# Optimization experiments

Hardware: AMD Instinct MI355X
Metric: run time of the kernel (lower is better)

Reference implementation:

```python
import jax, jax.numpy as jnp
import numpy as np

BN_EPS = 1e-5
INTERP_EPS = 1e-8


def setup_inputs() -> dict:
    key = jax.random.key(0)
    ks = jax.random.split(key, 8)
    B, N, S, D1, D2 = 8, 8192, 2048, 128, 256
    C_in, C_mid, C_out = D1 + D2, 256, 256
    return {
        "xyz1": jax.random.normal(ks[0], (B, 3, N), dtype=jnp.float32),
        "xyz2": jax.random.normal(ks[1], (B, 3, S), dtype=jnp.float32),
        "points1": jax.random.normal(ks[2], (B, D1, N), dtype=jnp.float32),
        "points2": jax.random.normal(ks[3], (B, D2, S), dtype=jnp.float32),
        "W0": jax.random.normal(ks[4], (C_mid, C_in), dtype=jnp.float32) * (1.0 / np.sqrt(C_in)),
        "b0": jnp.zeros((C_mid,), dtype=jnp.float32),
        "gamma0": jnp.ones((C_mid,), dtype=jnp.float32),
        "beta0": jnp.zeros((C_mid,), dtype=jnp.float32),
        "W1": jax.random.normal(ks[5], (C_out, C_mid), dtype=jnp.float32) * (1.0 / np.sqrt(C_mid)),
        "b1": jnp.zeros((C_out,), dtype=jnp.float32),
    }


def reference(xyz1, xyz2, points1, points2, W0, b0, gamma0, beta0, W1, b1):
    B, _, N = xyz1.shape
    S = xyz2.shape[2]
    x1 = jnp.transpose(xyz1, (0, 2, 1))  # (B, N, 3)
    x2 = jnpp = jnp.transpose(xyz2, (0, 2, 1))  # (B, S, 3)
    # squared distances: (B, N, S)
    d = (jnp.sum(x1 ** 2, -1)[:, :, None]
         + jnp.sum(x2 ** 2, -1)[:, None, :]
         - 2.0 * jnp.einsum('bnc,bsc->bns', x1, x2))
    # 3 nearest neighbors (fused top-3 instead of full sort; same math)
    neg_d, idx = jax.lax.top_k(-d, 3)  # (B, N, 3)
    dists = -neg_d
    recip = 1.0 / (dists + INTERP_EPS)
    weight = recip / jnp.sum(recip, axis=2, keepdims=True)  # (B, N, 3)
    p2t = jnp.transpose(points2, (0, 2, 1))  # (B, S, D2)
    D2 = p2t.shape[-1]
    gathered = jnp.take_along_axis(p2t, idx.reshape(B, N * 3, 1), axis=1).reshape(B, N, 3, D2)
    interp = jnp.einsum('bnkc,bnk->bcn', gathered, weight)  # (B, D2, N)
    new_points = jnp.concatenate([interp, points1], axis=1)  # (B, D2+D1, N)
    # conv0 (1x1) + BatchNorm (train mode, batch stats) + ReLU
    h = jnp.einsum('oc,bcn->bon', W0, new_points) + b0[None, :, None]
    mean = jnp.mean(h, axis=(0, 2), keepdims=True)
    var = jnp.mean((h - mean) ** 2, axis=(0, 2), keepdims=True)  # biased, as torch BN
    h = gamma0[None, :, None] * (h - mean) * jax.lax.rsqrt(var + BN_EPS) + beta0[None, :, None]
    h = jax.nn.relu(h)
    # conv1 (1x1) + Identity (module pairs conv1 with nn.Identity) + ReLU
    h = jnp.einsum('oc,bcn->bon', W1, h) + b1[None, :, None]
    return jax.nn.relu(h)
```

## Files before the change

kernel.cpp:

```cpp
#include <hip/hip_runtime.h>
#include <stdint.h>

constexpr int B = 8, N = 8192, S = 2048, D1 = 128, D2 = 256;
constexpr int CIN = 384, CMID = 256, COUT = 256;

typedef __attribute__((ext_vector_type(8))) _Float16 half8;
typedef __attribute__((ext_vector_type(4))) _Float16 half4;
typedef __attribute__((ext_vector_type(4))) float f32x4;

union HU { uint32_t u; _Float16 h[2]; };


__global__ __launch_bounds__(256) void k_top3(const float* __restrict__ xyz1,
                                              const float* __restrict__ xyz2,
                                              uint32_t* __restrict__ pw3) {
  __shared__ float4 Pq[S];
  __shared__ float md[4][3][128];
  __shared__ int mi[4][3][128];
  __shared__ float snrm[128];
  const int tid = threadIdx.x;
  const int wv = tid >> 6, lane = tid & 63;
  const int b = blockIdx.y;
  const int nb = blockIdx.x * 128;
  const float* x1 = xyz1 + (size_t)b * 3 * N;
  const float* x2 = xyz2 + (size_t)b * 3 * S;

  for (int j = tid; j < S; j += 256) {
    float sx = x2[j], sy = x2[j + S], sz = x2[j + 2 * S];
    Pq[j] = float4{sx, sy, sz, sx * sx + sy * sy + sz * sz};
  }
  float nax[2], nay[2], naz[2];
#pragma unroll
  for (int t = 0; t < 2; ++t) {
    const int n = nb + t * 64 + lane;
    const float ax = x1[n], ay = x1[n + N], az = x1[n + 2 * N];
    nax[t] = -2.f * ax; nay[t] = -2.f * ay; naz[t] = -2.f * az;
    if (wv == 0) snrm[t * 64 + lane] = ax * ax + ay * ay + az * az;
  }
  __syncthreads();

  float e0[2], e1[2], e2[2];
  int j0[2], j1[2], j2[2];
#pragma unroll
  for (int t = 0; t < 2; ++t) {
    e0[t] = 1e30f; e1[t] = 1e30f; e2[t] = 1e30f;
    j0[t] = 0; j1[t] = 0; j2[t] = 0;
  }
  const int s0 = wv * (S / 4), s1 = s0 + (S / 4);
#pragma unroll 4
  for (int s = s0; s < s1; ++s) {
    const float4 v = Pq[s];
#pragma unroll
    for (int t = 0; t < 2; ++t) {
      const float d = fmaf(nax[t], v.x, fmaf(nay[t], v.y, fmaf(naz[t], v.z, v.w)));
      const bool c0 = d < e0[t], c1 = d < e1[t], c2 = d < e2[t];
      const int u2 = c1 ? j1[t] : s;
      const int u1 = c0 ? j0[t] : s;
      j2[t] = c2 ? u2 : j2[t];
      j1[t] = c1 ? u1 : j1[t];
      j0[t] = c0 ? s : j0[t];
      e2[t] = __builtin_amdgcn_fmed3f(e1[t], e2[t], d);
      e1[t] = __builtin_amdgcn_fmed3f(e0[t], e1[t], d);
      e0[t] = fminf(e0[t], d);
    }
  }
#pragma unroll
  for (int t = 0; t < 2; ++t) {
    const int idx = t * 64 + lane;
    md[wv][0][idx] = e0[t]; mi[wv][0][idx] = j0[t];
    md[wv][1][idx] = e1[t]; mi[wv][1][idx] = j1[t];
    md[wv][2][idx] = e2[t]; mi[wv][2][idx] = j2[t];
  }
  __syncthreads();
  if (tid < 128) {
    float f0 = md[0][0][tid], f1 = md[0][1][tid], f2 = md[0][2][tid];
    int g0 = mi[0][0][tid], g1 = mi[0][1][tid], g2 = mi[0][2][tid];
#pragma unroll
    for (int w = 1; w < 4; ++w)
#pragma unroll
      for (int k = 0; k < 3; ++k) {
        float d = md[w][k][tid];
        int i = mi[w][k][tid];
        if (d < f2) {
          if (d < f1) {
            f2 = f1; g2 = g1;
            if (d < f0) { f1 = f0; g1 = g0; f0 = d; g0 = i; }
            else        { f1 = d;  g1 = i; }
          } else { f2 = d; g2 = i; }
        }
      }
    const float rn = snrm[tid];
    float q0 = fmaxf(f0 + rn, 0.f);
    float q1 = fmaxf(f1 + rn, 0.f);
    float q2 = fmaxf(f2 + rn, 0.f);
    float r0 = 1.0f / (q0 + 1e-8f), r1 = 1.0f / (q1 + 1e-8f), r2 = 1.0f / (q2 + 1e-8f);
    float inv = 1.0f / (r0 + r1 + r2);
    auto pack = [](int i, float w) -> uint32_t {
      uint32_t q = (uint32_t)(w * 2097152.0f + 0.5f);
      if (q > 0x1FFFFFu) q = 0x1FFFFFu;
      return ((uint32_t)i << 21) | q;
    };
    size_t base = ((size_t)b * N + nb + tid) * 3;
    pw3[base]     = pack(g0, r0 * inv);
    pw3[base + 1] = pack(g1, r1 * inv);
    pw3[base + 2] = pack(g2, r2 * inv);
  }
}

__global__ __launch_bounds__(256) void k_G(const float* __restrict__ points2,
                                           const float* __restrict__ W0,
                                           float* __restrict__ dout) {
  __shared__ half8 A_lds[4][256];
  __shared__ half8 B_lds[4][32];
  __shared__ float CT[32][258];
  const int tid = threadIdx.x;
  const int b = blockIdx.x >> 6;
  const int s0 = (blockIdx.x & 63) * 32;
  f32x4 acc[4][2] = {};
  const int wv = tid >> 6, lane = tid & 63;
  const int ln = lane & 15, quad = lane >> 4;
  const int bn = tid & 31, bkc = tid >> 5;
  const int ar = tid >> 3, ac4 = tid & 7;

  for (int kk = 0; kk < 256; kk += 32) {
    __syncthreads();
#pragma unroll
    for (int p = 0; p < 8; ++p) {
      int row = ar + 32 * p;
      const float4 v = *(const float4*)(W0 + (size_t)row * CIN + kk + ac4 * 4);
      half4 hv = {(_Float16)v.x, (_Float16)v.y, (_Float16)v.z, (_Float16)v.w};
      *(half4*)((_Float16*)&A_lds[ac4 >> 1][row] + (ac4 & 1) * 4) = hv;
    }
    {
      half4 hv;
#pragma unroll
      for (int j = 0; j < 4; ++j)
        hv[j] = (_Float16)points2[((size_t)(b * 256 + kk + bkc * 4 + j)) * S + s0 + bn];
      *(half4*)((_Float16*)&B_lds[bkc >> 1][bn] + (bkc & 1) * 4) = hv;
    }
    __syncthreads();
    half8 af[4], bf[2];
#pragma unroll
    for (int i = 0; i < 4; ++i) af[i] = A_lds[quad][wv * 64 + i * 16 + ln];
#pragma unroll
    for (int j = 0; j < 2; ++j) bf[j] = B_lds[quad][j * 16 + ln];
#pragma unroll
    for (int i = 0; i < 4; ++i)
#pragma unroll
      for (int j = 0; j < 2; ++j)
        acc[i][j] = __builtin_amdgcn_mfma_f32_16x16x32_f16(af[i], bf[j], acc[i][j], 0, 0, 0);
  }
  __syncthreads();
#pragma unroll
  for (int i = 0; i < 4; ++i)
#pragma unroll
    for (int reg = 0; reg < 4; ++reg) {
      int row = wv * 64 + i * 16 + quad * 4 + reg;
#pragma unroll
      for (int j = 0; j < 2; ++j) CT[j * 16 + ln][row] = acc[i][j][reg];
    }
  __syncthreads();
  const int sl = tid >> 3, g = tid & 7;
  float* g0 = dout + ((size_t)(b * 256 + 128)) * 8192 + (size_t)(s0 + sl) * 256 + g * 32;
#pragma unroll
  for (int q = 0; q < 8; ++q)
    *(float4*)(g0 + q * 4) = *(const float4*)&CT[sl][g * 32 + q * 4];
}

__global__ __launch_bounds__(256) void k_interp(const uint32_t* __restrict__ pw3,
                                                const float* __restrict__ dout_c,
                                                uint32_t* __restrict__ dout_u) {
  __shared__ int sidx[96];
  __shared__ float sw[96];
  const int tid = threadIdx.x;
  const int b = blockIdx.x >> 8;
  const int n0 = (blockIdx.x & 255) * 32;
  if (tid < 96) {
    uint32_t p = pw3[((size_t)b * N + n0) * 3 + tid];
    sidx[tid] = (int)(p >> 21);
    sw[tid] = (float)(p & 0x1FFFFFu) * (1.0f / 2097152.0f);
  }
  __syncthreads();
  const int colL = tid >> 3, p = tid & 7;
  const float* Gb = dout_c + ((size_t)(b * 256 + 128)) * 8192;
  float a[32];
#pragma unroll
  for (int q = 0; q < 32; ++q) a[q] = 0.f;
#pragma unroll
  for (int k = 0; k < 3; ++k) {
    int j = sidx[colL * 3 + k];
    float w = sw[colL * 3 + k];
    const float* g = Gb + (size_t)j * 256 + p * 32;
#pragma unroll
    for (int q = 0; q < 8; ++q) {
      float4 v = *(const float4*)(g + q * 4);
      a[q * 4 + 0] += w * v.x; a[q * 4 + 1] += w * v.y;
      a[q * 4 + 2] += w * v.z; a[q * 4 + 3] += w * v.w;
    }
  }
#pragma unroll
  for (int q = 0; q < 16; ++q) {
    int cp = p * 16 + q;
    HU u;
    u.h[0] = (_Float16)a[2 * q];
    u.h[1] = (_Float16)a[2 * q + 1];
    dout_u[((size_t)(b * 256 + cp)) * 8192 + n0 + colL] = u.u;
  }
}

__global__ __launch_bounds__(256) void k_wpack(const float* __restrict__ W0,
                                               const float* __restrict__ W1,
                                               _Float16* __restrict__ W1h,
                                               _Float16* __restrict__ W0h) {
  const int bid = blockIdx.x;
  if (bid < 64) {
    const int gid = bid * 256 + threadIdx.x;
    const float4 v = *(const float4*)(W1 + (size_t)gid * 4);
    half4 h = {(_Float16)v.x, (_Float16)v.y, (_Float16)v.z, (_Float16)v.w};
    *(half4*)(W1h + (size_t)gid * 4) = h;
  } else {
    const int gid = (bid - 64) * 256 + threadIdx.x;
    const int row = gid >> 5, c4 = gid & 31;
    const float4 v = *(const float4*)(W0 + (size_t)row * CIN + 256 + c4 * 4);
    half4 h = {(_Float16)v.x, (_Float16)v.y, (_Float16)v.z, (_Float16)v.w};
    *(half4*)(W0h + (size_t)row * 128 + c4 * 4) = h;
  }
}

__global__ __launch_bounds__(256) void k_h(uint32_t* __restrict__ h2,
                                           float* __restrict__ dpart,
                                           const float* __restrict__ points1,
                                           const _Float16* __restrict__ W0h,
                                           const float* __restrict__ b0) {
  __shared__ half8 B_lds[16][32];
  __shared__ float red_s[256], red_q[256], sb0[256];
  const int tid = threadIdx.x;
  const int b = blockIdx.x >> 8;
  const int cb = blockIdx.x & 255;
  const int n0 = cb * 32;
  sb0[tid] = b0[tid];
  const int wv = tid >> 6, lane = tid & 63;
  const int ln = lane & 15, quad = lane >> 4;

  f32x4 acc[4][2];
#pragma unroll
  for (int i = 0; i < 4; ++i) {
    const int rb = wv * 64 + i * 16 + quad * 4;
    const int cp0 = rb >> 1;
#pragma unroll
    for (int j = 0; j < 2; ++j) {
      const int col = n0 + j * 16 + ln;
      const size_t a0 = ((size_t)(b * 256 + cp0)) * 8192 + col;
      HU ua, ub;
      ua.u = h2[a0];
      ub.u = h2[a0 + 8192];
      acc[i][j][0] = (float)ua.h[0];
      acc[i][j][1] = (float)ua.h[1];
      acc[i][j][2] = (float)ub.h[0];
      acc[i][j][3] = (float)ub.h[1];
    }
  }
  {
    const int col = tid & 31;
    const int kc0 = tid >> 5;
#pragma unroll
    for (int it = 0; it < 2; ++it) {
      const int kc = kc0 + 8 * it;
      half8 hv;
#pragma unroll
      for (int j = 0; j < 8; ++j)
        hv[j] = (_Float16)points1[((size_t)(b * D1 + kc * 8 + j)) * N + n0 + col];
      B_lds[kc][col] = hv;
    }
  }
  __syncthreads();
  for (int kk = 0; kk < 128; kk += 32) {
    half8 af[4], bf[2];
#pragma unroll
    for (int i = 0; i < 4; ++i) {
      const int row = wv * 64 + i * 16 + ln;
      af[i] = *(const half8*)(W0h + (size_t)row * 128 + kk + quad * 8);
    }
#pragma unroll
    for (int j = 0; j < 2; ++j)
      bf[j] = B_lds[(kk >> 3) + quad][j * 16 + ln];
#pragma unroll
    for (int i = 0; i < 4; ++i)
#pragma unroll
      for (int j = 0; j < 2; ++j)
        acc[i][j] = __builtin_amdgcn_mfma_f32_16x16x32_f16(af[i], bf[j], acc[i][j], 0, 0, 0);
  }
#pragma unroll
  for (int i = 0; i < 4; ++i) {
    const int rb = wv * 64 + i * 16 + quad * 4;
    const int cp0 = rb >> 1;
    float rs[4] = {0.f, 0.f, 0.f, 0.f}, rq[4] = {0.f, 0.f, 0.f, 0.f};
#pragma unroll
    for (int j = 0; j < 2; ++j) {
      const int col = n0 + j * 16 + ln;
      const size_t a0 = ((size_t)(b * 256 + cp0)) * 8192 + col;
      _Float16 e0 = (_Float16)(acc[i][j][0] + sb0[rb + 0]);
      _Float16 e1 = (_Float16)(acc[i][j][1] + sb0[rb + 1]);
      _Float16 e2 = (_Float16)(acc[i][j][2] + sb0[rb + 2]);
      _Float16 e3 = (_Float16)(acc[i][j][3] + sb0[rb + 3]);
      HU o0, o1;
      o0.h[0] = e0; o0.h[1] = e1; o1.h[0] = e2; o1.h[1] = e3;
      h2[a0] = o0.u;
      h2[a0 + 8192] = o1.u;
      float f0 = (float)e0, f1 = (float)e1, f2 = (float)e2, f3 = (float)e3;
      rs[0] += f0; rq[0] += f0 * f0;
      rs[1] += f1; rq[1] += f1 * f1;
      rs[2] += f2; rq[2] += f2 * f2;
      rs[3] += f3; rq[3] += f3 * f3;
    }
#pragma unroll
    for (int reg = 0; reg < 4; ++reg) {
      float s = rs[reg], q = rq[reg];
#pragma unroll
      for (int m = 1; m < 16; m <<= 1) {
        s += __shfl_xor(s, m);
        q += __shfl_xor(q, m);
      }
      if (ln == 0) { red_s[rb + reg] = s; red_q[rb + reg] = q; }
    }
  }
  __syncthreads();
  float* part = dpart + ((size_t)(b * 256 + 192)) * 8192 + (size_t)cb * 512;
  part[tid] = red_s[tid];
  part[256 + tid] = red_q[tid];
}

__global__ __launch_bounds__(256) void k_bn(const float* __restrict__ dpart,
                                            const float* __restrict__ gamma,
                                            const float* __restrict__ beta,
                                            float* __restrict__ bna,
                                            float* __restrict__ bnb) {
  const int c = blockIdx.x;
  const int tid = threadIdx.x;
  float s = 0.f, q = 0.f;
#pragma unroll
  for (int u = tid; u < 2048; u += 256) {
    int b = u >> 8, cb = u & 255;
    const float* part = dpart + ((size_t)(b * 256 + 192)) * 8192 + (size_t)cb * 512;
    s += part[c];
    q += part[256 + c];
  }
#pragma unroll
  for (int m = 1; m < 64; m <<= 1) {
    s += __shfl_xor(s, m);
    q += __shfl_xor(q, m);
  }
  __shared__ float ls[4], lq[4];
  if ((tid & 63) == 0) { ls[tid >> 6] = s; lq[tid >> 6] = q; }
  __syncthreads();
  if (tid == 0) {
    float st = ls[0] + ls[1] + ls[2] + ls[3];
    float qt = lq[0] + lq[1] + lq[2] + lq[3];
    const float invn = 1.0f / (float)(B * N);
    float mean = st * invn;
    float var = qt * invn - mean * mean;
    float a = gamma[c] * rsqrtf(var + 1e-5f);
    bna[c] = a;
    bnb[c] = beta[c] - mean * a;
  }
}

__global__ __launch_bounds__(256) void k_fused1(const uint32_t* h2,
                                                const _Float16* __restrict__ W1h,
                                                const float* __restrict__ b1,
                                                const float* __restrict__ bna,
                                                const float* __restrict__ bnb,
                                                float* out) {
  __shared__ uint32_t Hh[32 * 33 * 4];
  __shared__ float sa[256], sb[256], sb1[256];
  const int tid = threadIdx.x;
  const int b = blockIdx.x >> 8;
  const int n0 = (blockIdx.x & 255) * 32;
  sa[tid] = bna[tid]; sb[tid] = bnb[tid]; sb1[tid] = b1[tid];
  __syncthreads();
  {
    const int c4 = tid & 7;
    const int rg = tid >> 3;
#pragma unroll
    for (int q = 0; q < 4; ++q) {
      const int cp = rg + 32 * q;
      const uint4 v = *(const uint4*)&h2[((size_t)(b * 256 + cp)) * 8192 + n0 + c4 * 4];
      const int k0 = 2 * cp;
      const float a0 = sa[k0], a1 = sa[k0 + 1], b0v = sb[k0], b1v = sb[k0 + 1];
      const int kc = cp >> 2, sub = cp & 3;
      const uint32_t vv[4] = {v.x, v.y, v.z, v.w};
#pragma unroll
      for (int m = 0; m < 4; ++m) {
        HU u; u.u = vv[m];
        float v0 = a0 * (float)u.h[0] + b0v;
        float v1 = a1 * (float)u.h[1] + b1v;
        HU o;
        o.h[0] = (_Float16)(v0 > 0.f ? v0 : 0.f);
        o.h[1] = (_Float16)(v1 > 0.f ? v1 : 0.f);
        Hh[((kc * 33) + c4 * 4 + m) * 4 + sub] = o.u;
      }
    }
  }
  __syncthreads();
  f32x4 acc[4][2] = {};
  const int wv = tid >> 6, lane = tid & 63;
  const int ln = lane & 15, quad = lane >> 4;
  for (int kk = 0; kk < 256; kk += 32) {
    half8 af[4], bf[2];
#pragma unroll
    for (int i = 0; i < 4; ++i) {
      int row = wv * 64 + i * 16 + ln;
      af[i] = *(const half8*)(W1h + (size_t)row * CMID + kk + quad * 8);
    }
#pragma unroll
    for (int j = 0; j < 2; ++j)
      bf[j] = *(const half8*)&Hh[(((kk >> 3) + quad) * 33 + j * 16 + ln) * 4];
#pragma unroll
    for (int i = 0; i < 4; ++i)
#pragma unroll
      for (int j = 0; j < 2; ++j)
        acc[i][j] = __builtin_amdgcn_mfma_f32_16x16x32_f16(af[i], bf[j], acc[i][j], 0, 0, 0);
  }
#pragma unroll
  for (int i = 0; i < 4; ++i) {
    const int rb = wv * 64 + i * 16 + quad * 4;
#pragma unroll
    for (int reg = 0; reg < 4; ++reg) {
      int row = rb + reg;
      float bias = sb1[row];
      float* orow = out + ((size_t)(b * 256 + row)) * 8192 + n0;
#pragma unroll
      for (int j = 0; j < 2; ++j)
        orow[j * 16 + ln] = fmaxf(acc[i][j][reg] + bias, 0.f);
    }
  }
}

extern "C" void kernel_launch(void* const* d_in, const int* in_sizes, int n_in,
                              void* d_out, int out_size, void* d_ws, size_t ws_size,
                              hipStream_t stream) {
  const float* xyz1 = (const float*)d_in[0];
  const float* xyz2 = (const float*)d_in[1];
  const float* points1 = (const float*)d_in[2];
  const float* points2 = (const float*)d_in[3];
  const float* W0 = (const float*)d_in[4];
  const float* b0 = (const float*)d_in[5];
  const float* gamma0 = (const float*)d_in[6];
  const float* beta0 = (const float*)d_in[7];
  const float* W1 = (const float*)d_in[8];
  const float* b1 = (const float*)d_in[9];
  float* out = (float*)d_out;

  char* ws = (char*)d_ws;
  float* bna = (float*)ws;
  float* bnb = (float*)(ws + 1024);
  uint32_t* pw3 = (uint32_t*)(ws + 2048);
  _Float16* W1h = (_Float16*)(ws + 2048);
  _Float16* W0h = (_Float16*)(ws + 2048 + 131072);

  k_top3<<<dim3(N / 128, B), 256, 0, stream>>>(xyz1, xyz2, pw3);
  k_G<<<dim3(B * 64), 256, 0, stream>>>(points2, W0, out);
  k_interp<<<dim3(B * N / 32), 256, 0, stream>>>(pw3, out, (uint32_t*)out);
  k_wpack<<<dim3(96), 256, 0, stream>>>(W0, W1, W1h, W0h);
  k_h<<<dim3(B * N / 32), 256, 0, stream>>>((uint32_t*)out, out, points1, W0h, b0);
  k_bn<<<dim3(256), 256, 0, stream>>>(out, gamma0, beta0, bna, bnb);
  k_fused1<<<dim3(B * N / 32), 256, 0, stream>>>((const uint32_t*)out, W1h, b1,
                                                 bna, bnb, out);
}
```

Measured before the change: 309.9 us.

## Precompute packed xyz2 float4 in global scratch and read directly in top-3 kernel

A new prep kernel writes (x,y,z,|p|^2) float4 records for every xyz2 point into a scratch region of the output buffer. The top-3 kernel then reads those records straight from global/L2 memory instead of staging all 2048 points into LDS in every block. Each thread now handles one query point instead of two, and the grid doubles so there are more blocks. This drops the per-block LDS fill and its barrier, and raises occupancy by shrinking LDS use. In exchange, every wave streams the point list through the cache hierarchy, and the scratch region in out must not be overwritten before k_top3 finishes reading it.

After: 332.5 us. 1.07x slower.

```diff
diff --git a/kernel.cpp b/kernel.cpp
--- a/kernel.cpp
+++ b/kernel.cpp
@@ -11,68 +11,54 @@
 union HU { uint32_t u; _Float16 h[2]; };
 
 
+__global__ __launch_bounds__(256) void k_prep(const float* __restrict__ xyz2,
+                                              float* __restrict__ dout) {
+  const int gid = blockIdx.x * 256 + threadIdx.x;
+  const int b = gid >> 11, s = gid & 2047;
+  const float* x2 = xyz2 + (size_t)b * 3 * S;
+  const float sx = x2[s], sy = x2[s + S], sz = x2[s + 2 * S];
+  float4 v = {sx, sy, sz, sx * sx + sy * sy + sz * sz};
+  *(float4*)(dout + ((size_t)(b * 256 + 208)) * 8192 + (size_t)s * 4) = v;
+}
+
 __global__ __launch_bounds__(256) void k_top3(const float* __restrict__ xyz1,
-                                              const float* __restrict__ xyz2,
+                                              const float* __restrict__ dP4,
                                               uint32_t* __restrict__ pw3) {
-  __shared__ float4 Pq[S];
-  __shared__ float md[4][3][128];
-  __shared__ int mi[4][3][128];
-  __shared__ float snrm[128];
+  __shared__ float md[4][3][64];
+  __shared__ int mi[4][3][64];
+  __shared__ float snrm[64];
   const int tid = threadIdx.x;
   const int wv = tid >> 6, lane = tid & 63;
   const int b = blockIdx.y;
-  const int nb = blockIdx.x * 128;
+  const int n = blockIdx.x * 64 + lane;
   const float* x1 = xyz1 + (size_t)b * 3 * N;
-  const float* x2 = xyz2 + (size_t)b * 3 * S;
-
-  for (int j = tid; j < S; j += 256) {
-    float sx = x2[j], sy = x2[j + S], sz = x2[j + 2 * S];
-    Pq[j] = float4{sx, sy, sz, sx * sx + sy * sy + sz * sz};
-  }
-  float nax[2], nay[2], naz[2];
-#pragma unroll
-  for (int t = 0; t < 2; ++t) {
-    const int n = nb + t * 64 + lane;
-    const float ax = x1[n], ay = x1[n + N], az = x1[n + 2 * N];
-    nax[t] = -2.f * ax; nay[t] = -2.f * ay; naz[t] = -2.f * az;
-    if (wv == 0) snrm[t * 64 + lane] = ax * ax + ay * ay + az * az;
-  }
-  __syncthreads();
-
-  float e0[2], e1[2], e2[2];
-  int j0[2], j1[2], j2[2];
-#pragma unroll
-  for (int t = 0; t < 2; ++t) {
-    e0[t] = 1e30f; e1[t] = 1e30f; e2[t] = 1e30f;
-    j0[t] = 0; j1[t] = 0; j2[t] = 0;
-  }
+  const float ax = x1[n], ay = x1[n + N], az = x1[n + 2 * N];
+  const float* P4 = dP4 + ((size_t)(b * 256 + 208)) * 8192;
+  if (wv == 0) snrm[lane] = ax * ax + ay * ay + az * az;
+
+  const float nax = -2.f * ax, nay = -2.f * ay, naz = -2.f * az;
+  float e0 = 1e30f, e1 = 1e30f, e2 = 1e30f;
+  int j0 = 0, j1 = 0, j2 = 0;
   const int s0 = wv * (S / 4), s1 = s0 + (S / 4);
-#pragma unroll 4
+#pragma unroll 8
   for (int s = s0; s < s1; ++s) {
-    const float4 v = Pq[s];
-#pragma unroll
-    for (int t = 0; t < 2; ++t) {
-      const float d = fmaf(nax[t], v.x, fmaf(nay[t], v.y, fmaf(naz[t], v.z, v.w)));
-      const bool c0 = d < e0[t], c1 = d < e1[t], c2 = d < e2[t];
-      const int u2 = c1 ? j1[t] : s;
-      const int u1 = c0 ? j0[t] : s;
-      j2[t] = c2 ? u2 : j2[t];
-      j1[t] = c1 ? u1 : j1[t];
-      j0[t] = c0 ? s : j0[t];
-      e2[t] = __builtin_amdgcn_fmed3f(e1[t], e2[t], d);
-      e1[t] = __builtin_amdgcn_fmed3f(e0[t], e1[t], d);
-      e0[t] = fminf(e0[t], d);
-    }
-  }
-#pragma unroll
-  for (int t = 0; t < 2; ++t) {
-    const int idx = t * 64 + lane;
-    md[wv][0][idx] = e0[t]; mi[wv][0][idx] = j0[t];
-    md[wv][1][idx] = e1[t]; mi[wv][1][idx] = j1[t];
-    md[wv][2][idx] = e2[t]; mi[wv][2][idx] = j2[t];
-  }
-  __syncthreads();
-  if (tid < 128) {
+    const float4 v = *(const float4*)(P4 + (size_t)s * 4);
+    const float d = fmaf(nax, v.x, fmaf(nay, v.y, fmaf(naz, v.z, v.w)));
+    const bool c0 = d < e0, c1 = d < e1, c2 = d < e2;
+    const int u2 = c1 ? j1 : s;
+    const int u1 = c0 ? j0 : s;
+    j2 = c2 ? u2 : j2;
+    j1 = c1 ? u1 : j1;
+    j0 = c0 ? s : j0;
+    e2 = __builtin_amdgcn_fmed3f(e1, e2, d);
+    e1 = __builtin_amdgcn_fmed3f(e0, e1, d);
+    e0 = fminf(e0, d);
+  }
+  md[wv][0][lane] = e0; mi[wv][0][lane] = j0;
+  md[wv][1][lane] = e1; mi[wv][1][lane] = j1;
+  md[wv][2][lane] = e2; mi[wv][2][lane] = j2;
+  __syncthreads();
+  if (tid < 64) {
     float f0 = md[0][0][tid], f1 = md[0][1][tid], f2 = md[0][2][tid];
     int g0 = mi[0][0][tid], g1 = mi[0][1][tid], g2 = mi[0][2][tid];
 #pragma unroll
@@ -100,7 +86,7 @@
       if (q > 0x1FFFFFu) q = 0x1FFFFFu;
       return ((uint32_t)i << 21) | q;
     };
-    size_t base = ((size_t)b * N + nb + tid) * 3;
+    size_t base = ((size_t)b * N + blockIdx.x * 64 + tid) * 3;
     pw3[base]     = pack(g0, r0 * inv);
     pw3[base + 1] = pack(g1, r1 * inv);
     pw3[base + 2] = pack(g2, r2 * inv);
@@ -458,7 +444,8 @@
   _Float16* W1h = (_Float16*)(ws + 2048);
   _Float16* W0h = (_Float16*)(ws + 2048 + 131072);
 
-  k_top3<<<dim3(N / 128, B), 256, 0, stream>>>(xyz1, xyz2, pw3);
+  k_prep<<<dim3(B * S / 256), 256, 0, stream>>>(xyz2, out);
+  k_top3<<<dim3(N / 64, B), 256, 0, stream>>>(xyz1, out, pw3);
   k_G<<<dim3(B * 64), 256, 0, stream>>>(points2, W0, out);
   k_interp<<<dim3(B * N / 32), 256, 0, stream>>>(pw3, out, (uint32_t*)out);
   k_wpack<<<dim3(96), 256, 0, stream>>>(W0, W1, W1h, W0h);
```
